# Optimization experiments

Hardware: AMD Instinct MI355X
Metric: run time of the kernel (lower is better)

The kernel has to match this reference:

```python
import jax, jax.numpy as jnp
import numpy as np

N, L, D = 8, 2048, 128


def setup_inputs() -> dict:
    key = jax.random.key(0)
    k1, k2, k3, k4 = jax.random.split(key, 4)
    x_t = jax.random.normal(k1, (N, L, D), jnp.float32)
    x_f = jax.random.normal(k2, (N, L, D), jnp.float32)
    W = jax.random.normal(k3, (D, D), jnp.float32) / np.sqrt(D)  # proj weight (torch Linear layout)
    b = jax.random.normal(k4, (D,), jnp.float32) * 0.02
    return {"x_t": x_t, "x_f": x_f, "W": W, "b": b}


def _col_score(a, c, scale):
    # softmax attention with zeroed diagonal, then column-sum -> [N, L]
    att = jnp.einsum('nld,nmd->nlm', a, c) * scale
    att = jax.nn.softmax(att, axis=-1)
    att = att * (1.0 - jnp.eye(att.shape[-1], dtype=att.dtype))
    return jnp.sum(att, axis=1)


def _mask(score, time):
    # score: [N, L]; k-th extreme threshold, k = L//2
    k = int(0.5 * score.shape[1])
    if time:
        vals, _ = jax.lax.top_k(score, k)          # k largest, descending
        theta = vals[:, -1:]                        # k-th largest
        return score > theta
    else:
        vals, _ = jax.lax.top_k(-score, k)          # k smallest
        theta = -vals[:, -1:]                       # k-th smallest
        return score <= theta


def reference(x_t, x_f, W, b):
    scale = 1.0 / np.sqrt(W.shape[0])
    pt = x_t @ W.T + b
    pf = x_f @ W.T + b
    score_t = _col_score(pt, pt, scale)
    score_f = _col_score(pf, pf, scale)
    score_tf = _col_score(pt, pf, scale)
    score_ft = _col_score(pf, pt, scale)
    mask_t = _mask(score_t, False)
    mask_f = _mask(score_f, False)
    mask_tf = _mask(score_tf, True)   # computed in original forward (unused in blend)
    mask_ft = _mask(score_ft, True)
    mask_t1 = (mask_t & ~mask_f)[:, :, None]   # [N, L, 1] broadcast over D
    mask_f1 = (mask_f & ~mask_t)[:, :, None]
    x_t1 = jnp.where(mask_t1, x_f, x_t)
    x_f1 = jnp.where(mask_f1, x_t, x_f)
    return (0.5 * (x_t1 + x_t), 0.5 * (x_f1 + x_f))
```

## Files before the change

### kernel.cpp

```cpp
#include <hip/hip_runtime.h>
#include <math.h>

#define LL 2048
#define DD 128
#define NS 16
#define SLAB (LL * DD)
#define SCALE 0.08838834764831845f

typedef __attribute__((ext_vector_type(8))) short short8v;
typedef __attribute__((ext_vector_type(4))) float float4v;

__device__ __forceinline__ unsigned int f2bf(float f) {
    unsigned int u = __float_as_uint(f);
    u += 0x7fffu + ((u >> 16) & 1u);
    return u >> 16;
}

__device__ __forceinline__ void strip_decode(int bx, int by, int& ib, int& ns) {
    const int lin = by * 16 + bx;
    const int xcd = lin & 7;
    const int w   = lin >> 3;
    ns = xcd + 8 * (w & 1);
    ib = w >> 1;
}

__device__ __forceinline__ void gl_lds16(const void* g, void* l) {
    __builtin_amdgcn_global_load_lds(
        (const __attribute__((address_space(1))) void*)g,
        (__attribute__((address_space(3))) void*)l, 16, 0, 0);
}

__device__ __forceinline__ void stage512(
    const unsigned short* __restrict__ gT, unsigned short* lbuf, int tid)
{
    const int row = tid >> 2;
    const int oc  = (tid & 3) ^ ((row >> 1) & 3);
    const int sb  = tid & ~63;
    gl_lds16(gT + (size_t)row * DD + oc * 8, lbuf + (size_t)sb * 8);
}

#define STAGE_HALF(DST, GH, GL, KC) do {                       \
    stage512((GH) + (KC) * 32,       (DST)[0], tid);           \
    stage512((GL) + (KC) * 32,       (DST)[1], tid);           \
    stage512((GH) + ((KC) + 1) * 32, (DST)[2], tid);           \
    stage512((GL) + ((KC) + 1) * 32, (DST)[3], tid); } while (0)

#define ZEROACC(ACC) do {                                      \
    _Pragma("unroll") for (int rt = 0; rt < 4; ++rt)           \
    _Pragma("unroll") for (int ct = 0; ct < 2; ++ct)           \
    _Pragma("unroll") for (int r = 0; r < 4; ++r) (ACC)[rt][ct][r] = 0.f; } while (0)

#define KC2(ACC, CB, KI, AKC) do {                                            \
    const unsigned short* BhP = (CB)[2 * (KI)];                               \
    const unsigned short* BlP = (CB)[2 * (KI) + 1];                           \
    short8v bh[2], bl[2], alv[4];                                             \
    _Pragma("unroll")                                                         \
    for (int ct = 0; ct < 2; ++ct) {                                          \
        const int r = wc * 32 + ct * 16 + l16;                                \
        const int off = r * 32 + ((quad ^ ((r >> 1) & 3)) << 3);              \
        bh[ct] = *(const short8v*)&BhP[off];                                  \
        bl[ct] = *(const short8v*)&BlP[off];                                  \
    }                                                                         \
    _Pragma("unroll")                                                         \
    for (int rt = 0; rt < 4; ++rt) {                                          \
        const int r = wr * 64 + rt * 16 + l16;                                \
        const int off = r * 32 + ((quad ^ ((r >> 1) & 3)) << 3);              \
        alv[rt] = *(const short8v*)&Alpan[AKC][off];                          \
    }                                                                         \
    __builtin_amdgcn_s_setprio(1);                                            \
    _Pragma("unroll")                                                         \
    for (int rt = 0; rt < 4; ++rt)                                            \
    _Pragma("unroll")                                                         \
    for (int ct = 0; ct < 2; ++ct) {                                          \
        (ACC)[rt][ct] = __builtin_amdgcn_mfma_f32_16x16x32_bf16(ah[AKC][rt], bh[ct], (ACC)[rt][ct], 0, 0, 0); \
        (ACC)[rt][ct] = __builtin_amdgcn_mfma_f32_16x16x32_bf16(ah[AKC][rt], bl[ct], (ACC)[rt][ct], 0, 0, 0); \
        (ACC)[rt][ct] = __builtin_amdgcn_mfma_f32_16x16x32_bf16(alv[rt],     bh[ct], (ACC)[rt][ct], 0, 0, 0); \
    }                                                                         \
    __builtin_amdgcn_s_setprio(0); } while (0)

#define EPI1(ACC) do {                                         \
    _Pragma("unroll") for (int rt = 0; rt < 4; ++rt)           \
    _Pragma("unroll") for (int rg = 0; rg < 4; ++rg) {         \
        float e0 = __expf((ACC)[rt][0][rg] * SCALE);           \
        float e1 = __expf((ACC)[rt][1][rg] * SCALE);           \
        z[rt][rg] += e0 + e1; } } while (0)

#define EPI2(ACC, JBV) do {                                    \
    float colp0 = 0.f, colp1 = 0.f;                            \
    const bool dgj = ((JBV) == ib);                            \
    _Pragma("unroll") for (int rt = 0; rt < 4; ++rt)           \
    _Pragma("unroll") for (int rg = 0; rg < 4; ++rg) {         \
        const int rl = wr * 64 + rt * 16 + quad * 4 + rg;      \
        float e0 = __expf((ACC)[rt][0][rg] * SCALE);           \
        float e1 = __expf((ACC)[rt][1][rg] * SCALE);           \
        bool s0 = dgj && (rl == wc * 32 + l16);                \
        bool s1 = dgj && (rl == wc * 32 + 16 + l16);           \
        colp0 += s0 ? 0.f : e0 * wrow[rt][rg];                 \
        colp1 += s1 ? 0.f : e1 * wrow[rt][rg]; }               \
    colp0 += __shfl_xor(colp0, 16); colp0 += __shfl_xor(colp0, 32); \
    colp1 += __shfl_xor(colp1, 16); colp1 += __shfl_xor(colp1, 32); \
    if (quad == 0) {                                           \
        scs[(JBV) * 128 + wc * 32 + l16][wr]      = colp0;     \
        scs[(JBV) * 128 + wc * 32 + 16 + l16][wr] = colp1; } } while (0)

__global__ __launch_bounds__(256, 4) void proj_kernel(
    const float* __restrict__ xt, const float* __restrict__ xf,
    const float* __restrict__ W,  const float* __restrict__ bias,
    unsigned short* __restrict__ Ph, unsigned short* __restrict__ Pl)
{
    __shared__ float Alds[64 * 36];
    __shared__ float Blds[128 * 36];
    __shared__ float bs[128];
    const int ns = blockIdx.y;
    const int l0 = blockIdx.x * 64;
    const int src = ns >> 3, n = ns & 7;
    const float* x = (src ? xf : xt) + (size_t)n * LL * DD;
    const int tid = threadIdx.x;
    const int ty = tid >> 4, tx = tid & 15;

    if (tid < 128) bs[tid] = bias[tid];
    __syncthreads();

    float acc[4][8];
#pragma unroll
    for (int i = 0; i < 4; ++i)
#pragma unroll
        for (int j = 0; j < 8; ++j) acc[i][j] = bs[tx + 16 * j];

    for (int kc = 0; kc < 4; ++kc) {
        __syncthreads();
#pragma unroll
        for (int t = 0; t < 2; ++t) {
            int idx = tid + t * 256;
            int r = idx >> 3, k4 = (idx & 7) << 2;
            *(float4*)&Alds[r * 36 + k4] =
                *(const float4*)&x[(size_t)(l0 + r) * DD + kc * 32 + k4];
        }
#pragma unroll
        for (int t = 0; t < 4; ++t) {
            int idx = tid + t * 256;
            int r = idx >> 3, k4 = (idx & 7) << 2;
            *(float4*)&Blds[r * 36 + k4] =
                *(const float4*)&W[(size_t)r * DD + kc * 32 + k4];
        }
        __syncthreads();
#pragma unroll
        for (int k4 = 0; k4 < 32; k4 += 4) {
            float4 a4[4], b4[8];
#pragma unroll
            for (int i = 0; i < 4; ++i) a4[i] = *(const float4*)&Alds[(ty + 16 * i) * 36 + k4];
#pragma unroll
            for (int j = 0; j < 8; ++j) b4[j] = *(const float4*)&Blds[(tx + 16 * j) * 36 + k4];
#pragma unroll
            for (int i = 0; i < 4; ++i)
#pragma unroll
                for (int j = 0; j < 8; ++j) {
                    acc[i][j] = fmaf(a4[i].x, b4[j].x, acc[i][j]);
                    acc[i][j] = fmaf(a4[i].y, b4[j].y, acc[i][j]);
                    acc[i][j] = fmaf(a4[i].z, b4[j].z, acc[i][j]);
                    acc[i][j] = fmaf(a4[i].w, b4[j].w, acc[i][j]);
                }
        }
    }
#pragma unroll
    for (int i = 0; i < 4; ++i) {
        const size_t rowo = (size_t)ns * SLAB + (size_t)(l0 + ty + 16 * i) * DD;
#pragma unroll
        for (int j = 0; j < 8; ++j) {
            float p = acc[i][j];
            unsigned int hb = f2bf(p);
            float hf = __uint_as_float(hb << 16);
            unsigned int lb = f2bf(p - hf);
            Ph[rowo + tx + 16 * j] = (unsigned short)hb;
            Pl[rowo + tx + 16 * j] = (unsigned short)lb;
        }
    }
}

__global__ __launch_bounds__(512, 2) void score_kernel(
    const unsigned short* __restrict__ Ph, const unsigned short* __restrict__ Pl,
    float* __restrict__ Spart)
{
    __shared__ unsigned short pan[2][4][4096];
    __shared__ unsigned short Alpan[4][4096];
    __shared__ float scs[2048][2];
    __shared__ float zl[128][4];
    int ib, ns;  strip_decode(blockIdx.x, blockIdx.y, ib, ns);
    const int tid = threadIdx.x;
    const int lane = tid & 63, quad = lane >> 4, l16 = lane & 15, wave = tid >> 6;
    const int wr = wave >> 2, wc = wave & 3;

    const unsigned short* sAh = Ph + (size_t)ns * SLAB + (size_t)ib * 128 * DD;
    const unsigned short* sAl = Pl + (size_t)ns * SLAB + (size_t)ib * 128 * DD;
    const unsigned short* sBh = Ph + (size_t)ns * SLAB;
    const unsigned short* sBl = Pl + (size_t)ns * SLAB;

    stage512(sAl,      Alpan[0], tid);
    stage512(sAl + 32, Alpan[1], tid);
    stage512(sAl + 64, Alpan[2], tid);
    stage512(sAl + 96, Alpan[3], tid);
    STAGE_HALF(pan[0], sBh, sBl, 0);
    short8v ah[4][4];
#pragma unroll
    for (int kc = 0; kc < 4; ++kc)
#pragma unroll
        for (int rt = 0; rt < 4; ++rt)
            ah[kc][rt] = *(const short8v*)
                &sAh[(size_t)(wr * 64 + rt * 16 + l16) * DD + kc * 32 + quad * 8];
    __syncthreads();

    float4v accA[4][2], accB[4][2];
    float z[4][4];
#pragma unroll
    for (int rt = 0; rt < 4; ++rt)
#pragma unroll
        for (int rg = 0; rg < 4; ++rg) z[rt][rg] = 0.f;

#pragma unroll 1
    for (int jp = 0; jp < 8; ++jp) {
        const unsigned short* b0h = sBh + (size_t)(2 * jp) * 128 * DD;
        const unsigned short* b0l = sBl + (size_t)(2 * jp) * 128 * DD;
        const unsigned short* b1h = b0h + 128 * DD;
        const unsigned short* b1l = b0l + 128 * DD;
        const unsigned short* b2h = b1h + 128 * DD;
        const unsigned short* b2l = b1l + 128 * DD;

        ZEROACC(accA);
        STAGE_HALF(pan[1], b0h, b0l, 2);
        KC2(accA, pan[0], 0, 0);
        KC2(accA, pan[0], 1, 1);
        if (jp) EPI1(accB);
        __syncthreads();

        STAGE_HALF(pan[0], b1h, b1l, 0);
        KC2(accA, pan[1], 0, 2);
        KC2(accA, pan[1], 1, 3);
        __syncthreads();

        ZEROACC(accB);
        STAGE_HALF(pan[1], b1h, b1l, 2);
        KC2(accB, pan[0], 0, 0);
        KC2(accB, pan[0], 1, 1);
        EPI1(accA);
        __syncthreads();

        if (jp < 7) STAGE_HALF(pan[0], b2h, b2l, 0);
        KC2(accB, pan[1], 0, 2);
        KC2(accB, pan[1], 1, 3);
        __syncthreads();
    }
    EPI1(accB);

#pragma unroll
    for (int rt = 0; rt < 4; ++rt)
#pragma unroll
        for (int rg = 0; rg < 4; ++rg) {
            float s = z[rt][rg];
            s += __shfl_xor(s, 1);
            s += __shfl_xor(s, 2);
            s += __shfl_xor(s, 4);
            s += __shfl_xor(s, 8);
            if (l16 == 0) zl[wr * 64 + rt * 16 + quad * 4 + rg][wc] = s;
        }
    STAGE_HALF(pan[0], sBh, sBl, 0);
    __syncthreads();
    float wrow[4][4];
#pragma unroll
    for (int rt = 0; rt < 4; ++rt)
#pragma unroll
        for (int rg = 0; rg < 4; ++rg) {
            const int row = wr * 64 + rt * 16 + quad * 4 + rg;
            wrow[rt][rg] = 1.0f / (zl[row][0] + zl[row][1] + zl[row][2] + zl[row][3]);
        }

#pragma unroll 1
    for (int jp = 0; jp < 8; ++jp) {
        const unsigned short* b0h = sBh + (size_t)(2 * jp) * 128 * DD;
        const unsigned short* b0l = sBl + (size_t)(2 * jp) * 128 * DD;
        const unsigned short* b1h = b0h + 128 * DD;
        const unsigned short* b1l = b0l + 128 * DD;
        const unsigned short* b2h = b1h + 128 * DD;
        const unsigned short* b2l = b1l + 128 * DD;

        ZEROACC(accA);
        STAGE_HALF(pan[1], b0h, b0l, 2);
        KC2(accA, pan[0], 0, 0);
        KC2(accA, pan[0], 1, 1);
        if (jp) EPI2(accB, 2 * jp - 1);
        __syncthreads();

        STAGE_HALF(pan[0], b1h, b1l, 0);
        KC2(accA, pan[1], 0, 2);
        KC2(accA, pan[1], 1, 3);
        __syncthreads();

        ZEROACC(accB);
        STAGE_HALF(pan[1], b1h, b1l, 2);
        KC2(accB, pan[0], 0, 0);
        KC2(accB, pan[0], 1, 1);
        EPI2(accA, 2 * jp);
        __syncthreads();

        if (jp < 7) STAGE_HALF(pan[0], b2h, b2l, 0);
        KC2(accB, pan[1], 0, 2);
        KC2(accB, pan[1], 1, 3);
        __syncthreads();
    }
    EPI2(accB, 15);

    __syncthreads();
#pragma unroll
    for (int g = 0; g < 4; ++g) {
        const int m = tid + g * 512;
        Spart[((size_t)ns * LL + m) * 16 + ib] = scs[m][0] + scs[m][1];
    }
}

__global__ __launch_bounds__(512) void mask_kernel(
    const float* __restrict__ Spart, unsigned char* __restrict__ maskbuf)
{
    __shared__ double s[LL];
    const int ns = blockIdx.x;
    const int q4 = blockIdx.y;
    const int tid = threadIdx.x;
#pragma unroll
    for (int g = 0; g < 4; ++g) {
        int m = tid + g * 512;
        const float* sp = Spart + ((size_t)ns * LL + m) * 16;
        double a = 0.0;
#pragma unroll
        for (int t = 0; t < 16; ++t) a += (double)sp[t];
        s[m] = a;
    }
    __syncthreads();
    const int i = q4 * 512 + tid;
    const double si = s[i];
    const double2* sv = (const double2*)s;
    int cnt = 0;
#pragma unroll 4
    for (int j = 0; j < LL / 2; ++j) {
        double2 p = sv[j];
        cnt += (p.x < si) ? 1 : 0;
        cnt += (p.y < si) ? 1 : 0;
    }
    maskbuf[ns * LL + i] = (cnt < 1024) ? 1 : 0;
}

__global__ __launch_bounds__(256) void blend_kernel(
    const float* __restrict__ xt, const float* __restrict__ xf,
    const unsigned char* __restrict__ maskbuf, float* __restrict__ out)
{
    const int idx4 = blockIdx.x * 256 + threadIdx.x;
    const size_t q = (size_t)idx4 * 4;
    const int row = (int)(q >> 7);
    const float4 a = *(const float4*)(xt + q);
    const float4 b = *(const float4*)(xf + q);
    const int mt = maskbuf[row] & 1;
    const int mf = maskbuf[16384 + row] & 1;
    const bool ct = mt && !mf;
    const bool cf = mf && !mt;
    float4 av;
    av.x = 0.5f * (a.x + b.x);  av.y = 0.5f * (a.y + b.y);
    av.z = 0.5f * (a.z + b.z);  av.w = 0.5f * (a.w + b.w);
    float4 o0 = ct ? av : a;
    float4 o1 = cf ? av : b;
    *(float4*)(out + q)                   = o0;
    *(float4*)(out + (size_t)2097152 + q) = o1;
}

extern "C" void kernel_launch(void* const* d_in, const int* in_sizes, int n_in,
                              void* d_out, int out_size, void* d_ws, size_t ws_size,
                              hipStream_t stream)
{
    const float* xt = (const float*)d_in[0];
    const float* xf = (const float*)d_in[1];
    const float* W  = (const float*)d_in[2];
    const float* b  = (const float*)d_in[3];
    float* out = (float*)d_out;

    unsigned short* Ph = (unsigned short*)d_out;
    unsigned short* Pl = Ph + (size_t)NS * SLAB;

    float* Spart = (float*)d_ws;
    unsigned char* maskbuf = (unsigned char*)(Spart + (size_t)16 * LL * 16);

    proj_kernel<<<dim3(32, NS), 256, 0, stream>>>(xt, xf, W, b, Ph, Pl);
    score_kernel<<<dim3(16, 16), 512, 0, stream>>>(Ph, Pl, Spart);
    mask_kernel<<<dim3(NS, 4), 512, 0, stream>>>(Spart, maskbuf);
    blend_kernel<<<2048, 256, 0, stream>>>(xt, xf, maskbuf, out);
}
```

Before: 220.1 us.

## Load full W and 128-row X tile into LDS with direct global-to-LDS copies

The projection kernel now stages the whole 128x128 weight matrix and a 128-row input tile into LDS in one pass, using gl_lds16 direct global-to-LDS loads with an XOR swizzle in place of padded rows. This removes the four K-chunk loop and its repeated barriers. Blocks grow to 512 threads covering 128 rows, which halves the grid. The cost is 128 KB of LDS per block, which limits occupancy to one block per CU, and the projection is only a small part of the total pipeline.

```diff
diff --git a/kernel.cpp b/kernel.cpp
--- a/kernel.cpp
+++ b/kernel.cpp
@@ -103,68 +103,63 @@
         scs[(JBV) * 128 + wc * 32 + l16][wr]      = colp0;     \
         scs[(JBV) * 128 + wc * 32 + 16 + l16][wr] = colp1; } } while (0)
 
-__global__ __launch_bounds__(256, 4) void proj_kernel(
+__global__ __launch_bounds__(512) void proj_kernel(
     const float* __restrict__ xt, const float* __restrict__ xf,
     const float* __restrict__ W,  const float* __restrict__ bias,
     unsigned short* __restrict__ Ph, unsigned short* __restrict__ Pl)
 {
-    __shared__ float Alds[64 * 36];
-    __shared__ float Blds[128 * 36];
-    __shared__ float bs[128];
+    __shared__ float Wl[128 * 128];
+    __shared__ float Xl[128 * 128];
     const int ns = blockIdx.y;
-    const int l0 = blockIdx.x * 64;
+    const int l0 = blockIdx.x * 128;
     const int src = ns >> 3, n = ns & 7;
-    const float* x = (src ? xf : xt) + (size_t)n * LL * DD;
+    const float* x = (src ? xf : xt) + (size_t)n * LL * DD + (size_t)l0 * DD;
     const int tid = threadIdx.x;
     const int ty = tid >> 4, tx = tid & 15;
 
-    if (tid < 128) bs[tid] = bias[tid];
-    __syncthreads();
+#pragma unroll
+    for (int it = 0; it < 8; ++it) {
+        const int s   = it * 512 + tid;
+        const int row = s >> 5, c = s & 31;
+        const int oc  = c ^ (row & 7);
+        const int sb  = it * 512 + (tid & ~63);
+        gl_lds16(W + (size_t)row * DD + oc * 4, Wl + (size_t)sb * 4);
+        gl_lds16(x + (size_t)row * DD + oc * 4, Xl + (size_t)sb * 4);
+    }
 
     float acc[4][8];
 #pragma unroll
     for (int i = 0; i < 4; ++i)
 #pragma unroll
-        for (int j = 0; j < 8; ++j) acc[i][j] = bs[tx + 16 * j];
-
-    for (int kc = 0; kc < 4; ++kc) {
-        __syncthreads();
-#pragma unroll
-        for (int t = 0; t < 2; ++t) {
-            int idx = tid + t * 256;
-            int r = idx >> 3, k4 = (idx & 7) << 2;
-            *(float4*)&Alds[r * 36 + k4] =
-                *(const float4*)&x[(size_t)(l0 + r) * DD + kc * 32 + k4];
-        }
-#pragma unroll
-        for (int t = 0; t < 4; ++t) {
-            int idx = tid + t * 256;
-            int r = idx >> 3, k4 = (idx & 7) << 2;
-            *(float4*)&Blds[r * 36 + k4] =
-                *(const float4*)&W[(size_t)r * DD + kc * 32 + k4];
-        }
-        __syncthreads();
-#pragma unroll
-        for (int k4 = 0; k4 < 32; k4 += 4) {
-            float4 a4[4], b4[8];
-#pragma unroll
-            for (int i = 0; i < 4; ++i) a4[i] = *(const float4*)&Alds[(ty + 16 * i) * 36 + k4];
-#pragma unroll
-            for (int j = 0; j < 8; ++j) b4[j] = *(const float4*)&Blds[(tx + 16 * j) * 36 + k4];
-#pragma unroll
-            for (int i = 0; i < 4; ++i)
-#pragma unroll
-                for (int j = 0; j < 8; ++j) {
-                    acc[i][j] = fmaf(a4[i].x, b4[j].x, acc[i][j]);
-                    acc[i][j] = fmaf(a4[i].y, b4[j].y, acc[i][j]);
-                    acc[i][j] = fmaf(a4[i].z, b4[j].z, acc[i][j]);
-                    acc[i][j] = fmaf(a4[i].w, b4[j].w, acc[i][j]);
-                }
-        }
-    }
+        for (int j = 0; j < 8; ++j) acc[i][j] = bias[tx + 16 * j];
+
+    __syncthreads();
+
+    const int rs = ty & 7, ds = tx & 7;
+#pragma unroll 4
+    for (int k4 = 0; k4 < 128; k4 += 4) {
+        const int c = k4 >> 2;
+        float4 xv[4], wv[8];
+#pragma unroll
+        for (int i = 0; i < 4; ++i)
+            xv[i] = *(const float4*)&Xl[(ty + 32 * i) * 128 + ((c ^ rs) << 2)];
+#pragma unroll
+        for (int j = 0; j < 8; ++j)
+            wv[j] = *(const float4*)&Wl[(tx + 16 * j) * 128 + ((c ^ ds) << 2)];
+#pragma unroll
+        for (int i = 0; i < 4; ++i)
+#pragma unroll
+            for (int j = 0; j < 8; ++j) {
+                acc[i][j] = fmaf(xv[i].x, wv[j].x, acc[i][j]);
+                acc[i][j] = fmaf(xv[i].y, wv[j].y, acc[i][j]);
+                acc[i][j] = fmaf(xv[i].z, wv[j].z, acc[i][j]);
+                acc[i][j] = fmaf(xv[i].w, wv[j].w, acc[i][j]);
+            }
+    }
+
 #pragma unroll
     for (int i = 0; i < 4; ++i) {
-        const size_t rowo = (size_t)ns * SLAB + (size_t)(l0 + ty + 16 * i) * DD;
+        const size_t rowo = (size_t)ns * SLAB + (size_t)(l0 + ty + 32 * i) * DD;
 #pragma unroll
         for (int j = 0; j < 8; ++j) {
             float p = acc[i][j];
@@ -384,7 +379,7 @@
     float* Spart = (float*)d_ws;
     unsigned char* maskbuf = (unsigned char*)(Spart + (size_t)16 * LL * 16);
 
-    proj_kernel<<<dim3(32, NS), 256, 0, stream>>>(xt, xf, W, b, Ph, Pl);
+    proj_kernel<<<dim3(16, NS), 512, 0, stream>>>(xt, xf, W, b, Ph, Pl);
     score_kernel<<<dim3(16, 16), 512, 0, stream>>>(Ph, Pl, Spart);
     mask_kernel<<<dim3(NS, 4), 512, 0, stream>>>(Spart, maskbuf);
     blend_kernel<<<2048, 256, 0, stream>>>(xt, xf, maskbuf, out);
```

After: 220.4 us. About the same (+0.2%).
